# Performance work log

Measured on AMD Instinct MI355X. Metric: run time of the kernel, lower is better.

Reference implementation:

```python
import jax, jax.numpy as jnp
import numpy as np

T = 256          # trellis length (steps per sequence)
L = 16           # state bits
K = 2            # code bits per step
V = 2            # weights emitted per step
TLUT_BITS = 10   # LUT index bits
OUT, IN = 4096, 4096
NSEQ = (OUT * IN) // (T * V)      # 32768
CODES_PER_WORD = 32 // K          # 16


def fwht(x):
    """Normalized fast Walsh-Hadamard transform along the last axis (power-of-2)."""
    n = x.shape[-1]
    lead = x.shape[:-1]
    h = 1
    while h < n:
        x = x.reshape(lead + (n // (2 * h), 2, h))
        a, b = x[..., 0, :], x[..., 1, :]
        x = jnp.stack([a + b, a - b], axis=-2).reshape(lead + (n,))
        h *= 2
    return x / jnp.sqrt(jnp.asarray(n, x.dtype))


def decode_trellis(trellis, tlut):
    """Bit-unpack K-bit transition codes, run the L-bit shift-register trellis,
    and look up V weight values per state in the LUT."""
    t = jnp.arange(T)
    words = trellis[:, t // CODES_PER_WORD]            # [NSEQ, T] int32
    shifts = (32 - K) - K * (t % CODES_PER_WORD)       # MSB-first unpack
    codes = (words >> shifts) & (2 ** K - 1)           # [NSEQ, T]

    def step(state, code):
        state = ((state << K) | code) & (2 ** L - 1)
        return state, state

    _, states = jax.lax.scan(step, jnp.zeros(trellis.shape[0], jnp.int32),
                             codes.T.astype(jnp.int32))  # states: [T, NSEQ]
    states = states.T                                   # [NSEQ, T]
    vals = tlut[states & (2 ** TLUT_BITS - 1)]          # [NSEQ, T, V] LUT gather
    return vals.reshape(OUT, IN)


def incoherence_process(w_hat, SU, SV):
    """W = diag(SV) H_out  W_hat  H_in diag(SU)  (random-sign Hadamard)."""
    w = fwht(w_hat)        # Hadamard along in-dim
    w = fwht(w.T).T        # Hadamard along out-dim
    return w * SV[:, None] * SU[None, :]


def setup_inputs() -> dict:
    key = jax.random.key(0)
    ks = jax.random.split(key, 5)
    x = jax.random.normal(ks[0], (8192, IN), jnp.float32)
    trellis = jax.random.randint(ks[1], (NSEQ, 32 * T * K // (32 * 32)) if False else (NSEQ, (T * K) // 32), 0, 2147483647, dtype=jnp.int32)
    tlut = jax.random.normal(ks[2], (2 ** TLUT_BITS, V), jnp.float32)
    SU = jnp.sign(jax.random.normal(ks[3], (IN,), jnp.float32)) * 0.02
    SV = jnp.sign(jax.random.normal(ks[4], (OUT,), jnp.float32)) * 0.02
    return {"x": x, "trellis": trellis, "tlut": tlut, "SU": SU, "SV": SV}


def reference(x, trellis, tlut, SU, SV):
    w_hat = decode_trellis(trellis, tlut)       # [OUT, IN] dequantized weight
    w = incoherence_process(w_hat, SU, SV)      # Hadamard incoherence undo
    return x @ w.T                              # F.linear
```

## Files before the change

kernel.cpp:

```cpp
#include <hip/hip_runtime.h>
#include <hip/hip_bf16.h>
#include <stdint.h>

typedef __bf16 bf16x8 __attribute__((ext_vector_type(8)));
typedef float  f32x4  __attribute__((ext_vector_type(4)));

#define IN_DIM  4096
#define OUT_DIM 4096
#define M_DIM   8192

#define AS1 __attribute__((address_space(1)))
#define AS3 __attribute__((address_space(3)))

static __device__ __forceinline__ void gload_lds16(const void* g, void* l) {
  __builtin_amdgcn_global_load_lds((const AS1 void*)g, (AS3 void*)l, 16, 0, 0);
}

__global__ __launch_bounds__(256) void k_decode_fwht_row(
    const int* __restrict__ trellis, const float2* __restrict__ tlut,
    const float* __restrict__ SU, __hip_bfloat16* __restrict__ w)
{
  __shared__ float buf[4096];
  __shared__ int words[128];
  __shared__ float2 lut[1024];
  const int tid = threadIdx.x;
  const int r = blockIdx.x;

  if (tid < 128) words[tid] = trellis[r * 128 + tid];
  for (int i = tid; i < 1024; i += 256) lut[i] = tlut[i];
  __syncthreads();

  {
    const int t  = tid;
    const int wi = t >> 4;
    const int sh = 30 - 2 * (t & 15);
    const unsigned mask = (t < 4) ? ((1u << (2 * t + 2)) - 1u) : 1023u;
    #pragma unroll
    for (int s = 0; s < 8; ++s) {
      unsigned lo = (unsigned)words[s * 16 + wi];
      unsigned hi = wi ? (unsigned)words[s * 16 + wi - 1] : 0u;
      unsigned long long comb = ((unsigned long long)hi << 32) | (unsigned long long)lo;
      unsigned st = ((unsigned)(comb >> sh)) & mask;
      float2 v = lut[st];
      buf[s * 512 + 2 * t]     = v.x + v.y;
      buf[s * 512 + 2 * t + 1] = v.x - v.y;
    }
  }
  __syncthreads();

  for (int h = 2; h < 4096; h <<= 1) {
    #pragma unroll
    for (int q = 0; q < 8; ++q) {
      int b = q * 256 + tid;
      int i = ((b & ~(h - 1)) << 1) | (b & (h - 1));
      float a = buf[i], c = buf[i + h];
      buf[i]     = a + c;
      buf[i + h] = a - c;
    }
    __syncthreads();
  }

  for (int q = 0; q < 16; ++q) {
    int c = q * 256 + tid;
    w[(size_t)r * IN_DIM + c] = __float2bfloat16(buf[c] * SU[c] * 0.015625f);
  }
}

__global__ __launch_bounds__(256) void k_fwht64_lo(__hip_bfloat16* __restrict__ w)
{
  __shared__ float tile[64][65];
  const int tid = threadIdx.x;
  const int rb = blockIdx.y, cb = blockIdx.x;

  for (int q = 0; q < 16; ++q) {
    int idx = q * 256 + tid;
    int rr = idx >> 6, cc = idx & 63;
    tile[rr][cc] = __bfloat162float(w[(size_t)(rb * 64 + rr) * IN_DIM + cb * 64 + cc]);
  }
  __syncthreads();

  const int c = tid & 63, qf = tid >> 6;
  for (int h = 1; h < 64; h <<= 1) {
    #pragma unroll
    for (int u = 0; u < 8; ++u) {
      int b = qf * 8 + u;
      int i = ((b & ~(h - 1)) << 1) | (b & (h - 1));
      float a = tile[i][c], d = tile[i + h][c];
      tile[i][c]     = a + d;
      tile[i + h][c] = a - d;
    }
    __syncthreads();
  }

  for (int q = 0; q < 16; ++q) {
    int idx = q * 256 + tid;
    int rr = idx >> 6, cc = idx & 63;
    w[(size_t)(rb * 64 + rr) * IN_DIM + cb * 64 + cc] = __float2bfloat16(tile[rr][cc]);
  }
}

__global__ __launch_bounds__(256) void k_fwht64_hi(__hip_bfloat16* __restrict__ w,
                                                   const float* __restrict__ SV)
{
  __shared__ float tile[64][65];
  const int tid = threadIdx.x;
  const int r0 = blockIdx.y, cb = blockIdx.x;

  for (int q = 0; q < 16; ++q) {
    int idx = q * 256 + tid;
    int r1 = idx >> 6, cc = idx & 63;
    tile[r1][cc] = __bfloat162float(w[(size_t)(r0 + 64 * r1) * IN_DIM + cb * 64 + cc]);
  }
  __syncthreads();

  const int c = tid & 63, qf = tid >> 6;
  for (int h = 1; h < 64; h <<= 1) {
    #pragma unroll
    for (int u = 0; u < 8; ++u) {
      int b = qf * 8 + u;
      int i = ((b & ~(h - 1)) << 1) | (b & (h - 1));
      float a = tile[i][c], d = tile[i + h][c];
      tile[i][c]     = a + d;
      tile[i + h][c] = a - d;
    }
    __syncthreads();
  }

  for (int q = 0; q < 16; ++q) {
    int idx = q * 256 + tid;
    int r1 = idx >> 6, cc = idx & 63;
    int row = r0 + 64 * r1;
    w[(size_t)row * IN_DIM + cb * 64 + cc] =
        __float2bfloat16(tile[r1][cc] * SV[row] * 0.015625f);
  }
}

__global__ __launch_bounds__(256) void k_cvt_x(const float* __restrict__ x,
                                               __hip_bfloat16* __restrict__ xb)
{
  size_t i = ((size_t)blockIdx.x * 256 + threadIdx.x) * 8;
  float4 v0 = *(const float4*)(x + i);
  float4 v1 = *(const float4*)(x + i + 4);
  union { __hip_bfloat16 h[8]; uint4 u; } p;
  p.h[0] = __float2bfloat16(v0.x); p.h[1] = __float2bfloat16(v0.y);
  p.h[2] = __float2bfloat16(v0.z); p.h[3] = __float2bfloat16(v0.w);
  p.h[4] = __float2bfloat16(v1.x); p.h[5] = __float2bfloat16(v1.y);
  p.h[6] = __float2bfloat16(v1.z); p.h[7] = __float2bfloat16(v1.w);
  *(uint4*)(xb + i) = p.u;
}

#define GBM 256
#define GBN 256
#define GBK 64
#define NT  (IN_DIM / GBK)

__global__ __launch_bounds__(512, 2) void k_gemm256(
    const __hip_bfloat16* __restrict__ X,
    const __hip_bfloat16* __restrict__ W,
    float* __restrict__ out)
{
  extern __shared__ __hip_bfloat16 smem[];
  __hip_bfloat16* As = smem;
  __hip_bfloat16* Bs = smem + 2 * 16384;

  const int tid  = threadIdx.x;
  const int lane = tid & 63;
  const int wave = tid >> 6;
  const int wm   = wave >> 2;
  const int wn   = wave & 3;
  const int lm   = lane & 15;
  const int lq   = lane >> 4;
  const int s_rw = tid >> 3;
  const int s_jj = tid & 7;

  const int nwg  = gridDim.x * gridDim.y;
  const int cpx  = nwg >> 3;
  const int orig = blockIdx.y * gridDim.x + blockIdx.x;
  const int swz  = (orig & 7) * cpx + (orig >> 3);
  const int bx   = swz % gridDim.x;
  const int by   = swz / gridDim.x;
  const int m0 = by * GBM, n0 = bx * GBN;

  f32x4 acc[8][4] = {};
  bf16x8 a_[4][2];
  bf16x8 b0_[2][2];
  bf16x8 b1_[2][2];

#define STAGE_A(buf, u, kt) do {                                              \
    int row_ = (u) * 64 + s_rw;                                               \
    int js_  = s_jj ^ (row_ & 7);                                             \
    gload_lds16(X + (size_t)(m0 + row_) * IN_DIM + (kt) * GBK + js_ * 8,      \
                As + (buf) * 16384 + row_ * 64 + s_jj * 8);                   \
  } while (0)
#define STAGE_BE(buf, half, kt) do {                                          \
    int row_ = (half) * 128 + (s_rw & 31) + ((s_rw & 32) << 1);               \
    int js_  = s_jj ^ (row_ & 7);                                             \
    gload_lds16(W + (size_t)(n0 + row_) * IN_DIM + (kt) * GBK + js_ * 8,      \
                Bs + (buf) * 16384 + row_ * 64 + s_jj * 8);                   \
  } while (0)
#define STAGE_BL(buf, half, kt) do {                                          \
    int row_ = (half) * 128 + 32 + (s_rw & 31) + ((s_rw & 32) << 1);          \
    int js_  = s_jj ^ (row_ & 7);                                             \
    gload_lds16(W + (size_t)(n0 + row_) * IN_DIM + (kt) * GBK + js_ * 8,      \
                Bs + (buf) * 16384 + row_ * 64 + s_jj * 8);                   \
  } while (0)

#define RD_A(QM, BUF) do {                                                    \
    const __hip_bfloat16* Ab_ = As + (BUF) * 16384;                           \
    _Pragma("unroll")                                                         \
    for (int mi2 = 0; mi2 < 4; ++mi2) {                                       \
      int r_ = wm * 128 + (QM) * 64 + mi2 * 16 + lm;                          \
      _Pragma("unroll")                                                       \
      for (int kk = 0; kk < 2; ++kk) {                                        \
        int q_ = kk * 4 + lq;                                                 \
        a_[mi2][kk] = *(const bf16x8*)(Ab_ + r_ * 64 + ((q_ ^ (r_ & 7)) << 3)); \
      }                                                                       \
    }                                                                         \
  } while (0)
#define RD_B(DST, QN, BUF) do {                                               \
    const __hip_bfloat16* Bb_ = Bs + (BUF) * 16384;                           \
    _Pragma("unroll")                                                         \
    for (int ni2 = 0; ni2 < 2; ++ni2) {                                       \
      int r_ = wn * 64 + (QN) * 32 + ni2 * 16 + lm;                           \
      _Pragma("unroll")                                                       \
      for (int kk = 0; kk < 2; ++kk) {                                        \
        int q_ = kk * 4 + lq;                                                 \
        DST[ni2][kk] = *(const bf16x8*)(Bb_ + r_ * 64 + ((q_ ^ (r_ & 7)) << 3)); \
      }                                                                       \
    }                                                                         \
  } while (0)

#define PH_MID do {                                                           \
    __builtin_amdgcn_s_barrier();                                             \
    asm volatile("s_waitcnt lgkmcnt(0)" ::: "memory");                        \
    __builtin_amdgcn_sched_barrier(0);                                        \
    __builtin_amdgcn_s_setprio(1);                                            \
  } while (0)
#define MFMA_Q(QM, QN, BF) do {                                               \
    _Pragma("unroll")                                                         \
    for (int mi2 = 0; mi2 < 4; ++mi2)                                         \
      _Pragma("unroll")                                                       \
      for (int ni2 = 0; ni2 < 2; ++ni2)                                       \
        _Pragma("unroll")                                                     \
        for (int kk = 0; kk < 2; ++kk)                                        \
          acc[(QM) * 4 + mi2][(QN) * 2 + ni2] =                               \
              __builtin_amdgcn_mfma_f32_16x16x32_bf16(                        \
                  a_[mi2][kk], BF[ni2][kk],                                   \
                  acc[(QM) * 4 + mi2][(QN) * 2 + ni2], 0, 0, 0);              \
  } while (0)
#define VM4   do { asm volatile("s_waitcnt vmcnt(4)" ::: "memory"); } while (0)
#define PH_END do {                                                           \
    __builtin_amdgcn_s_setprio(0);                                            \
    __builtin_amdgcn_s_barrier();                                             \
  } while (0)
#define PH_END_VM do {                                                        \
    __builtin_amdgcn_s_setprio(0);                                            \
    VM4;                                                                      \
    __builtin_amdgcn_s_barrier();                                             \
  } while (0)

  STAGE_BE(0, 0, 0); STAGE_BE(0, 1, 0);
  STAGE_A (0, 0, 0); STAGE_A (0, 2, 0);
  STAGE_BL(0, 0, 0); STAGE_BL(0, 1, 0);
  STAGE_A (0, 1, 0); STAGE_A (0, 3, 0);
  STAGE_A (1, 0, 1); STAGE_A (1, 2, 1);
  STAGE_BL(1, 0, 1); STAGE_BL(1, 1, 1);
  asm volatile("s_waitcnt vmcnt(4)" ::: "memory");
  __builtin_amdgcn_s_barrier();

  for (int it = 0; it < NT / 2; ++it) {
    const int t1 = 2 * it + 1;
    const int t2 = (2 * it + 2 < NT) ? 2 * it + 2 : NT - 1;
    const int t3 = (2 * it + 3 < NT) ? 2 * it + 3 : NT - 1;

    RD_A(0, 0); RD_B(b0_, 0, 0);
    STAGE_A(1, 1, t1); STAGE_A(1, 3, t1);
    PH_MID; MFMA_Q(0, 0, b0_); PH_END;
    RD_B(b1_, 1, 0);
    STAGE_BE(1, 0, t1); STAGE_BE(1, 1, t1);
    PH_MID; MFMA_Q(0, 1, b1_); PH_END;
    RD_A(1, 0);
    STAGE_A(0, 0, t2); STAGE_A(0, 2, t2);
    PH_MID; MFMA_Q(1, 1, b1_); PH_END;
    RD_B(b0_, 0, 0);
    STAGE_BL(0, 0, t2); STAGE_BL(0, 1, t2);
    PH_MID; MFMA_Q(1, 0, b0_); PH_END_VM;

    RD_A(0, 1); RD_B(b0_, 0, 1);
    STAGE_A(0, 1, t2); STAGE_A(0, 3, t2);
    PH_MID; MFMA_Q(0, 0, b0_); PH_END;
    RD_B(b1_, 1, 1);
    STAGE_BE(0, 0, t2); STAGE_BE(0, 1, t2);
    PH_MID; MFMA_Q(0, 1, b1_); PH_END;
    RD_A(1, 1);
    STAGE_A(1, 0, t3); STAGE_A(1, 2, t3);
    PH_MID; MFMA_Q(1, 1, b1_); PH_END;
    RD_B(b0_, 0, 1);
    STAGE_BL(1, 0, t3); STAGE_BL(1, 1, t3);
    PH_MID; MFMA_Q(1, 0, b0_); PH_END_VM;
  }

  #pragma unroll
  for (int mi = 0; mi < 8; ++mi) {
    #pragma unroll
    for (int ni = 0; ni < 4; ++ni) {
      int col   = n0 + wn * 64 + ni * 16 + lm;
      int rbase = m0 + wm * 128 + mi * 16 + lq * 4;
      #pragma unroll
      for (int rg = 0; rg < 4; ++rg) {
        out[(size_t)(rbase + rg) * OUT_DIM + col] = acc[mi][ni][rg];
      }
    }
  }
#undef PH_END_VM
#undef PH_END
#undef VM4
#undef MFMA_Q
#undef PH_MID
#undef RD_B
#undef RD_A
#undef STAGE_BL
#undef STAGE_BE
#undef STAGE_A
}

extern "C" void kernel_launch(void* const* d_in, const int* in_sizes, int n_in,
                              void* d_out, int out_size, void* d_ws, size_t ws_size,
                              hipStream_t stream) {
  (void)in_sizes; (void)n_in; (void)out_size; (void)ws_size;
  const float* x       = (const float*)d_in[0];
  const int*   trellis = (const int*)d_in[1];
  const float* tlut    = (const float*)d_in[2];
  const float* SU      = (const float*)d_in[3];
  const float* SV      = (const float*)d_in[4];
  float* out = (float*)d_out;

  __hip_bfloat16* Wd = (__hip_bfloat16*)d_ws;
  __hip_bfloat16* Xb = (__hip_bfloat16*)((char*)d_ws + (size_t)32 * 1024 * 1024);

  k_decode_fwht_row<<<4096, 256, 0, stream>>>(trellis, (const float2*)tlut, SU, Wd);
  k_fwht64_lo<<<dim3(64, 64), 256, 0, stream>>>(Wd);
  k_fwht64_hi<<<dim3(64, 64), 256, 0, stream>>>(Wd, SV);
  k_cvt_x<<<16384, 256, 0, stream>>>(x, Xb);

  hipFuncSetAttribute((const void*)k_gemm256,
                      hipFuncAttributeMaxDynamicSharedMemorySize, 131072);
  k_gemm256<<<dim3(IN_DIM / GBN, M_DIM / GBM), 512, 131072, stream>>>(Xb, Wd, out);
}
```

Before: 351.3 us.

## Vectorize bf16 FWHT loads/stores and let GEMM LDS reads overlap MFMAs

```diff
diff --git a/kernel.cpp b/kernel.cpp
--- a/kernel.cpp
+++ b/kernel.cpp
@@ -14,6 +14,12 @@
 
 static __device__ __forceinline__ void gload_lds16(const void* g, void* l) {
   __builtin_amdgcn_global_load_lds((const AS1 void*)g, (AS3 void*)l, 16, 0, 0);
+}
+static __device__ __forceinline__ float bf2f(unsigned short u) {
+  union { uint32_t i; float f; } c; c.i = (uint32_t)u << 16; return c.f;
+}
+static __device__ __forceinline__ unsigned short f2bf(float f) {
+  __hip_bfloat16 h = __float2bfloat16(f); return *(const unsigned short*)&h;
 }
 
 __global__ __launch_bounds__(256) void k_decode_fwht_row(
@@ -60,9 +66,13 @@
     __syncthreads();
   }
 
-  for (int q = 0; q < 16; ++q) {
-    int c = q * 256 + tid;
-    w[(size_t)r * IN_DIM + c] = __float2bfloat16(buf[c] * SU[c] * 0.015625f);
+  for (int it2 = 0; it2 < 2; ++it2) {
+    int c0 = (it2 * 256 + tid) * 8;
+    union { unsigned short us[8]; uint4 v; } p;
+    #pragma unroll
+    for (int e = 0; e < 8; ++e)
+      p.us[e] = f2bf(buf[c0 + e] * SU[c0 + e] * 0.015625f);
+    *(uint4*)(w + (size_t)r * IN_DIM + c0) = p.v;
   }
 }
 
@@ -72,10 +82,13 @@
   const int tid = threadIdx.x;
   const int rb = blockIdx.y, cb = blockIdx.x;
 
-  for (int q = 0; q < 16; ++q) {
-    int idx = q * 256 + tid;
-    int rr = idx >> 6, cc = idx & 63;
-    tile[rr][cc] = __bfloat162float(w[(size_t)(rb * 64 + rr) * IN_DIM + cb * 64 + cc]);
+  for (int it = 0; it < 2; ++it) {
+    int chunk = it * 256 + tid;
+    int rr = chunk >> 3, jc = chunk & 7;
+    uint4 v = *(const uint4*)(w + (size_t)(rb * 64 + rr) * IN_DIM + cb * 64 + jc * 8);
+    const unsigned short* u = (const unsigned short*)&v;
+    #pragma unroll
+    for (int e = 0; e < 8; ++e) tile[rr][jc * 8 + e] = bf2f(u[e]);
   }
   __syncthreads();
 
@@ -92,10 +105,13 @@
     __syncthreads();
   }
 
-  for (int q = 0; q < 16; ++q) {
-    int idx = q * 256 + tid;
-    int rr = idx >> 6, cc = idx & 63;
-    w[(size_t)(rb * 64 + rr) * IN_DIM + cb * 64 + cc] = __float2bfloat16(tile[rr][cc]);
+  for (int it = 0; it < 2; ++it) {
+    int chunk = it * 256 + tid;
+    int rr = chunk >> 3, jc = chunk & 7;
+    union { unsigned short us[8]; uint4 v; } p;
+    #pragma unroll
+    for (int e = 0; e < 8; ++e) p.us[e] = f2bf(tile[rr][jc * 8 + e]);
+    *(uint4*)(w + (size_t)(rb * 64 + rr) * IN_DIM + cb * 64 + jc * 8) = p.v;
   }
 }
 
@@ -106,10 +122,13 @@
   const int tid = threadIdx.x;
   const int r0 = blockIdx.y, cb = blockIdx.x;
 
-  for (int q = 0; q < 16; ++q) {
-    int idx = q * 256 + tid;
-    int r1 = idx >> 6, cc = idx & 63;
-    tile[r1][cc] = __bfloat162float(w[(size_t)(r0 + 64 * r1) * IN_DIM + cb * 64 + cc]);
+  for (int it = 0; it < 2; ++it) {
+    int chunk = it * 256 + tid;
+    int r1 = chunk >> 3, jc = chunk & 7;
+    uint4 v = *(const uint4*)(w + (size_t)(r0 + 64 * r1) * IN_DIM + cb * 64 + jc * 8);
+    const unsigned short* u = (const unsigned short*)&v;
+    #pragma unroll
+    for (int e = 0; e < 8; ++e) tile[r1][jc * 8 + e] = bf2f(u[e]);
   }
   __syncthreads();
 
@@ -126,12 +145,15 @@
     __syncthreads();
   }
 
-  for (int q = 0; q < 16; ++q) {
-    int idx = q * 256 + tid;
-    int r1 = idx >> 6, cc = idx & 63;
+  for (int it = 0; it < 2; ++it) {
+    int chunk = it * 256 + tid;
+    int r1 = chunk >> 3, jc = chunk & 7;
     int row = r0 + 64 * r1;
-    w[(size_t)row * IN_DIM + cb * 64 + cc] =
-        __float2bfloat16(tile[r1][cc] * SV[row] * 0.015625f);
+    float sv = SV[row] * 0.015625f;
+    union { unsigned short us[8]; uint4 v; } p;
+    #pragma unroll
+    for (int e = 0; e < 8; ++e) p.us[e] = f2bf(tile[r1][jc * 8 + e] * sv);
+    *(uint4*)(w + (size_t)row * IN_DIM + cb * 64 + jc * 8) = p.v;
   }
 }
 
@@ -182,9 +204,6 @@
   const int m0 = by * GBM, n0 = bx * GBN;
 
   f32x4 acc[8][4] = {};
-  bf16x8 a_[4][2];
-  bf16x8 b0_[2][2];
-  bf16x8 b1_[2][2];
 
 #define STAGE_A(buf, u, kt) do {                                              \
     int row_ = (u) * 64 + s_rw;                                               \
@@ -205,7 +224,7 @@
                 Bs + (buf) * 16384 + row_ * 64 + s_jj * 8);                   \
   } while (0)
 
-#define RD_A(QM, BUF) do {                                                    \
+#define RD_A_TO(DST, QM, BUF) do {                                            \
     const __hip_bfloat16* Ab_ = As + (BUF) * 16384;                           \
     _Pragma("unroll")                                                         \
     for (int mi2 = 0; mi2 < 4; ++mi2) {                                       \
@@ -213,11 +232,11 @@
       _Pragma("unroll")                                                       \
       for (int kk = 0; kk < 2; ++kk) {                                        \
         int q_ = kk * 4 + lq;                                                 \
-        a_[mi2][kk] = *(const bf16x8*)(Ab_ + r_ * 64 + ((q_ ^ (r_ & 7)) << 3)); \
+        DST[mi2][kk] = *(const bf16x8*)(Ab_ + r_ * 64 + ((q_ ^ (r_ & 7)) << 3)); \
       }                                                                       \
     }                                                                         \
   } while (0)
-#define RD_B(DST, QN, BUF) do {                                               \
+#define RD_B_TO(DST, QN, BUF) do {                                            \
     const __hip_bfloat16* Bb_ = Bs + (BUF) * 16384;                           \
     _Pragma("unroll")                                                         \
     for (int ni2 = 0; ni2 < 2; ++ni2) {                                       \
@@ -230,13 +249,10 @@
     }                                                                         \
   } while (0)
 
-#define PH_MID do {                                                           \
-    __builtin_amdgcn_s_barrier();                                             \
-    asm volatile("s_waitcnt lgkmcnt(0)" ::: "memory");                        \
-    __builtin_amdgcn_sched_barrier(0);                                        \
-    __builtin_amdgcn_s_setprio(1);                                            \
-  } while (0)
-#define MFMA_Q(QM, QN, BF) do {                                               \
+#define FENCE asm volatile("" ::: "memory")
+#define PH_BAR do { FENCE; __builtin_amdgcn_s_barrier(); FENCE;               \
+                    __builtin_amdgcn_s_setprio(1); } while (0)
+#define MFMA_Q2(QM, QN, AF, BF) do {                                          \
     _Pragma("unroll")                                                         \
     for (int mi2 = 0; mi2 < 4; ++mi2)                                         \
       _Pragma("unroll")                                                       \
@@ -245,19 +261,14 @@
         for (int kk = 0; kk < 2; ++kk)                                        \
           acc[(QM) * 4 + mi2][(QN) * 2 + ni2] =                               \
               __builtin_amdgcn_mfma_f32_16x16x32_bf16(                        \
-                  a_[mi2][kk], BF[ni2][kk],                                   \
+                  AF[mi2][kk], BF[ni2][kk],                                   \
                   acc[(QM) * 4 + mi2][(QN) * 2 + ni2], 0, 0, 0);              \
   } while (0)
-#define VM4   do { asm volatile("s_waitcnt vmcnt(4)" ::: "memory"); } while (0)
-#define PH_END do {                                                           \
-    __builtin_amdgcn_s_setprio(0);                                            \
-    __builtin_amdgcn_s_barrier();                                             \
-  } while (0)
-#define PH_END_VM do {                                                        \
-    __builtin_amdgcn_s_setprio(0);                                            \
-    VM4;                                                                      \
-    __builtin_amdgcn_s_barrier();                                             \
-  } while (0)
+#define VM4 do { asm volatile("s_waitcnt vmcnt(4)" ::: "memory"); } while (0)
+#define PH_END    do { __builtin_amdgcn_s_setprio(0); FENCE;                  \
+                       __builtin_amdgcn_s_barrier(); FENCE; } while (0)
+#define PH_END_VM do { __builtin_amdgcn_s_setprio(0); VM4;                    \
+                       __builtin_amdgcn_s_barrier(); FENCE; } while (0)
 
   STAGE_BE(0, 0, 0); STAGE_BE(0, 1, 0);
   STAGE_A (0, 0, 0); STAGE_A (0, 2, 0);
@@ -266,38 +277,39 @@
   STAGE_A (1, 0, 1); STAGE_A (1, 2, 1);
   STAGE_BL(1, 0, 1); STAGE_BL(1, 1, 1);
   asm volatile("s_waitcnt vmcnt(4)" ::: "memory");
-  __builtin_amdgcn_s_barrier();
+  __builtin_amdgcn_s_barrier(); FENCE;
 
   for (int it = 0; it < NT / 2; ++it) {
     const int t1 = 2 * it + 1;
     const int t2 = (2 * it + 2 < NT) ? 2 * it + 2 : NT - 1;
     const int t3 = (2 * it + 3 < NT) ? 2 * it + 3 : NT - 1;
 
-    RD_A(0, 0); RD_B(b0_, 0, 0);
+    bf16x8 aE[4][2], aO[4][2], b0[2][2], b1[2][2];
+    bf16x8 aE1[4][2], aO1[4][2], b01[2][2], b11[2][2];
+
+    RD_A_TO(aE, 0, 0); RD_B_TO(b0, 0, 0);
     STAGE_A(1, 1, t1); STAGE_A(1, 3, t1);
-    PH_MID; MFMA_Q(0, 0, b0_); PH_END;
-    RD_B(b1_, 1, 0);
+    PH_BAR; MFMA_Q2(0, 0, aE, b0); PH_END;
+    RD_B_TO(b1, 1, 0);
     STAGE_BE(1, 0, t1); STAGE_BE(1, 1, t1);
-    PH_MID; MFMA_Q(0, 1, b1_); PH_END;
-    RD_A(1, 0);
+    PH_BAR; MFMA_Q2(0, 1, aE, b1); PH_END;
+    RD_A_TO(aO, 1, 0);
     STAGE_A(0, 0, t2); STAGE_A(0, 2, t2);
-    PH_MID; MFMA_Q(1, 1, b1_); PH_END;
-    RD_B(b0_, 0, 0);
+    PH_BAR; MFMA_Q2(1, 1, aO, b1); PH_END;
     STAGE_BL(0, 0, t2); STAGE_BL(0, 1, t2);
-    PH_MID; MFMA_Q(1, 0, b0_); PH_END_VM;
-
-    RD_A(0, 1); RD_B(b0_, 0, 1);
+    PH_BAR; MFMA_Q2(1, 0, aO, b0); PH_END_VM;
+
+    RD_A_TO(aE1, 0, 1); RD_B_TO(b01, 0, 1);
     STAGE_A(0, 1, t2); STAGE_A(0, 3, t2);
-    PH_MID; MFMA_Q(0, 0, b0_); PH_END;
-    RD_B(b1_, 1, 1);
+    PH_BAR; MFMA_Q2(0, 0, aE1, b01); PH_END;
+    RD_B_TO(b11, 1, 1);
     STAGE_BE(0, 0, t2); STAGE_BE(0, 1, t2);
-    PH_MID; MFMA_Q(0, 1, b1_); PH_END;
-    RD_A(1, 1);
+    PH_BAR; MFMA_Q2(0, 1, aE1, b11); PH_END;
+    RD_A_TO(aO1, 1, 1);
     STAGE_A(1, 0, t3); STAGE_A(1, 2, t3);
-    PH_MID; MFMA_Q(1, 1, b1_); PH_END;
-    RD_B(b0_, 0, 1);
+    PH_BAR; MFMA_Q2(1, 1, aO1, b11); PH_END;
     STAGE_BL(1, 0, t3); STAGE_BL(1, 1, t3);
-    PH_MID; MFMA_Q(1, 0, b0_); PH_END_VM;
+    PH_BAR; MFMA_Q2(1, 0, aO1, b01); PH_END_VM;
   }
 
   #pragma unroll
@@ -315,10 +327,11 @@
 #undef PH_END_VM
 #undef PH_END
 #undef VM4
-#undef MFMA_Q
-#undef PH_MID
-#undef RD_B
-#undef RD_A
+#undef MFMA_Q2
+#undef PH_BAR
+#undef FENCE
+#undef RD_B_TO
+#undef RD_A_TO
 #undef STAGE_BL
 #undef STAGE_BE
 #undef STAGE_A
```

Measured after the change: 355.0 us. No clear change (+1.1%).
